# Kernel optimization log

Measured on AMD Instinct MI355X. Metric: run time of the kernel, lower is better.

The kernel has to match this reference:

```python
import jax, jax.numpy as jnp
import numpy as np

EPS = 1e-15          # min-norm clamp (matches torch min_norm)
BALL_EPS = 4e-3      # float32 Poincare ball boundary eps
C = 1.0              # curvature for every layer


def _artanh(x):
    x = jnp.clip(x, -1.0 + 1e-7, 1.0 - 1e-7)
    return 0.5 * jnp.log((1.0 + x) / (1.0 - x))


def _norm(x):
    return jnp.maximum(jnp.linalg.norm(x, axis=-1, keepdims=True), EPS)


def proj(x, c):
    # clip points to stay inside the ball of radius (1-eps)/sqrt(c)
    n = _norm(x)
    maxnorm = (1.0 - BALL_EPS) / jnp.sqrt(c)
    return jnp.where(n > maxnorm, x / n * maxnorm, x)


def expmap0(u, c):
    sc = jnp.sqrt(c)
    n = _norm(u)
    return jnp.tanh(sc * n) * u / (sc * n)


def logmap0(p, c):
    sc = jnp.sqrt(c)
    n = _norm(p)
    return _artanh(sc * n) * p / (sc * n)


def mobius_add(x, y, c):
    x2 = jnp.sum(x * x, axis=-1, keepdims=True)
    y2 = jnp.sum(y * y, axis=-1, keepdims=True)
    xy = jnp.sum(x * y, axis=-1, keepdims=True)
    num = (1.0 + 2.0 * c * xy + c * y2) * x + (1.0 - c * x2) * y
    den = 1.0 + 2.0 * c * xy + (c ** 2) * x2 * y2
    return num / jnp.maximum(den, EPS)


def mobius_matvec(W, x, c):
    # torch HypLinear: mx = x @ W.T
    sc = jnp.sqrt(c)
    xn = _norm(x)
    mx = x @ W.T
    mxn = _norm(mx)
    res = jnp.tanh(mxn / xn * _artanh(sc * xn)) * mx / (mxn * sc)
    zero = jnp.all(mx == 0.0, axis=-1, keepdims=True)
    return jnp.where(zero, jnp.zeros((), dtype=res.dtype), res)


def hgc_layer(h, src, dst, w, W, b, c_in, c_out, n_nodes):
    # HypLinear
    mv = proj(mobius_matvec(W, h, c_in), c_in)
    hb = proj(expmap0(b[None, :], c_in), c_in)
    h = proj(mobius_add(mv, hb, c_in), c_in)
    # HypAgg: spmm in the tangent space at the origin
    xt = logmap0(h, c_in)                                  # [N, D]
    msg = w[:, None] * xt[src]                             # [E, D]
    agg = jax.ops.segment_sum(msg, dst, num_segments=n_nodes)
    h = proj(expmap0(agg, c_in), c_in)
    # HypAct: relu in tangent space, re-map with c_out
    xt = jax.nn.relu(logmap0(h, c_in))
    return proj(expmap0(xt, c_out), c_out)


def setup_inputs() -> dict:
    key = jax.random.key(0)
    k = jax.random.split(key, 8)
    N, E, F, D = 80000, 1280000, 256, 64
    x = jax.random.normal(k[0], (N, F), dtype=jnp.float32)
    src = jax.random.randint(k[1], (E,), 0, N)
    dst = jax.random.randint(k[2], (E,), 0, N)
    edge_weight = jax.random.uniform(k[3], (E,), dtype=jnp.float32)
    W1 = jax.random.normal(k[4], (D, F), dtype=jnp.float32) / np.sqrt(F)
    b1 = jax.random.normal(k[5], (D,), dtype=jnp.float32) * 0.01
    W2 = jax.random.normal(k[6], (D, D), dtype=jnp.float32) / np.sqrt(D)
    b2 = jax.random.normal(k[7], (D,), dtype=jnp.float32) * 0.01
    return {"x": x, "src": src, "dst": dst, "edge_weight": edge_weight,
            "W1": W1, "b1": b1, "W2": W2, "b2": b2}


def reference(x, src, dst, edge_weight, W1, b1, W2, b2):
    n_nodes = x.shape[0]
    # encode(): proj_tan0 is identity on the Poincare ball
    h = proj(expmap0(x, C), C)
    h = hgc_layer(h, src, dst, edge_weight, W1, b1, C, C, n_nodes)
    h = hgc_layer(h, src, dst, edge_weight, W2, b2, C, C, n_nodes)
    return h
```

## Files before the change

kernel.cpp:

```cpp
#include <hip/hip_runtime.h>


#define EPSV 1e-15f
#define MAXN 0.996f

typedef unsigned short bfu;
typedef __attribute__((ext_vector_type(8))) short v8s;
typedef __attribute__((ext_vector_type(4))) float v4f;

__device__ __forceinline__ bfu f2b(float f) {
    unsigned int u;
    __builtin_memcpy(&u, &f, sizeof(u));
    u += 0x7fffu + ((u >> 16) & 1u);
    return (bfu)(u >> 16);
}

__device__ __forceinline__ float b2f(bfu s) {
    unsigned int u = ((unsigned int)s) << 16;
    float f;
    __builtin_memcpy(&f, &u, sizeof(f));
    return f;
}

__device__ __forceinline__ float uplo(unsigned int u) {
    unsigned int v = u << 16; float f;
    __builtin_memcpy(&f, &v, sizeof(f)); return f;
}
__device__ __forceinline__ float uphi(unsigned int u) {
    unsigned int v = u & 0xffff0000u; float f;
    __builtin_memcpy(&f, &v, sizeof(f)); return f;
}

__device__ __forceinline__ v8s cvt8(const float* f) {
    v8s r;
#pragma unroll
    for (int j = 0; j < 8; ++j) r[j] = (short)f2b(f[j]);
    return r;
}

__device__ __forceinline__ float i2f(int i) {
    float f; __builtin_memcpy(&f, &i, sizeof(f)); return f;
}
__device__ __forceinline__ int f2i(float f) {
    int i; __builtin_memcpy(&i, &f, sizeof(i)); return i;
}

__device__ __forceinline__ float wredsum(float v) {
#pragma unroll
    for (int o = 32; o > 0; o >>= 1) v += __shfl_xor(v, o, 64);
    return v;
}

__device__ __forceinline__ float artanh_(float x) {
    x = fminf(fmaxf(x, -1.0f + 1e-7f), 1.0f - 1e-7f);
    return 0.5f * logf((1.0f + x) / (1.0f - x));
}

__device__ __forceinline__ float mobius_tail(float mx, float xn, float hb, float y2) {
    float mxn2 = wredsum(mx * mx);
    unsigned long long nz = __ballot(mx != 0.0f);
    float mxn = fmaxf(sqrtf(mxn2), EPSV);
    float rt = tanhf(mxn / xn * artanh_(xn));
    float mv, x2s;
    if (nz != 0ull) {
        mv = (rt / mxn) * mx;
        float mvn = fmaxf(fabsf(rt), EPSV);
        if (mvn > MAXN) mv *= MAXN / mvn;
        float cn = fminf(mvn, MAXN);
        x2s = cn * cn;
    } else { mv = 0.0f; x2s = 0.0f; }
    float xy = wredsum(mv * hb);
    float ca = 1.0f + 2.0f * xy + y2;
    float cb = 1.0f - x2s;
    float den = fmaxf(1.0f + 2.0f * xy + x2s * y2, EPSV);
    float hj = (ca * mv + cb * hb) / den;
    float hn = fmaxf(sqrtf(wredsum(hj * hj)), EPSV);
    if (hn > MAXN) { hj *= MAXN / hn; hn = MAXN; }
    return (artanh_(hn) / hn) * hj;
}

__device__ __forceinline__ float agg_transform(float a, float* xn_out) {
    float n = fmaxf(sqrtf(wredsum(a * a)), EPSV);
    float th = tanhf(n);
    float g = th / n;
    float nh = fmaxf(th, EPSV);
    if (nh > MAXN) { g *= MAXN / nh; nh = MAXN; }
    float h = g * a;
    float t = fmaxf((artanh_(nh) / nh) * h, 0.0f);
    float n2 = fmaxf(sqrtf(wredsum(t * t)), EPSV);
    float th2 = tanhf(n2);
    float g2 = th2 / n2;
    float nh2 = fmaxf(th2, EPSV);
    if (nh2 > MAXN) { g2 *= MAXN / nh2; nh2 = MAXN; }
    *xn_out = nh2;
    return g2 * t;
}

__device__ __forceinline__ float bias_point(const float* bv, int lane, float* y2) {
    float b = bv[lane];
    float bn = fmaxf(sqrtf(wredsum(b * b)), EPSV);
    float gs = tanhf(bn) / bn;
    float hbn = fmaxf(tanhf(bn), EPSV);
    if (hbn > MAXN) gs *= MAXN / hbn;
    float hb = gs * b;
    *y2 = wredsum(hb * hb);
    return hb;
}

__global__ __launch_bounds__(256) void hgA_zero(float* __restrict__ p, int n4) {
    const float4 z = make_float4(0.f, 0.f, 0.f, 0.f);
    int stride = gridDim.x * blockDim.x;
    for (int i = blockIdx.x * blockDim.x + threadIdx.x; i < n4; i += stride)
        ((float4*)p)[i] = z;
}

__global__ __launch_bounds__(256) void hgA_prep(
    int* __restrict__ deg, int N,
    const float* __restrict__ W1, const float* __restrict__ W2,
    bfu* __restrict__ w1b, bfu* __restrict__ w2b, int NW1, int NW2)
{
    const int b = blockIdx.x, tid = threadIdx.x;
    if (b < 128) {
        for (int i = b * 256 + tid; i < N; i += 128 * 256) deg[i] = 0;
    } else if (b < 128 + (NW1 + 255) / 256) {
        int i = (b - 128) * 256 + tid;
        if (i < NW1) w1b[i] = f2b(W1[i]);
    } else {
        for (int i = tid; i < NW2; i += 256) w2b[i] = f2b(W2[i]);
    }
}

__device__ __forceinline__ void layer1_body(
    int bid, int tid, const float* __restrict__ x, const bfu* __restrict__ w1b,
    const float* __restrict__ b1v, bfu* __restrict__ xtb, int N)
{
    const int lane = tid & 63, wv = tid >> 6;
    const int nodeBase = (bid * 4 + wv) * 16;
    if (nodeBase >= N) return;

    float y2;
    float hb = bias_point(b1v, lane, &y2);
    float hbv[4];
#pragma unroll
    for (int t = 0; t < 4; ++t) hbv[t] = __shfl(hb, (lane & 15) + 16 * t);

    const int m = lane & 15, q = lane >> 4;
    v4f acc0 = {0,0,0,0}, acc1 = {0,0,0,0}, acc2 = {0,0,0,0}, acc3 = {0,0,0,0};
    float usq = 0.0f;

    const float* arow = x + (size_t)(nodeBase + m) * 256 + q * 8;
    const bfu* wrow = w1b + (size_t)m * 256 + q * 8;
#pragma unroll
    for (int s = 0; s < 8; ++s) {
        float af[8];
        *(float4*)(af)     = *(const float4*)(arow + s * 32);
        *(float4*)(af + 4) = *(const float4*)(arow + s * 32 + 4);
#pragma unroll
        for (int j = 0; j < 8; ++j) usq = fmaf(af[j], af[j], usq);
        v8s a = cvt8(af);
        const bfu* wb = wrow + s * 32;
        acc0 = __builtin_amdgcn_mfma_f32_16x16x32_bf16(a, *(const v8s*)(wb), acc0, 0, 0, 0);
        acc1 = __builtin_amdgcn_mfma_f32_16x16x32_bf16(a, *(const v8s*)(wb + 16 * 256), acc1, 0, 0, 0);
        acc2 = __builtin_amdgcn_mfma_f32_16x16x32_bf16(a, *(const v8s*)(wb + 32 * 256), acc2, 0, 0, 0);
        acc3 = __builtin_amdgcn_mfma_f32_16x16x32_bf16(a, *(const v8s*)(wb + 48 * 256), acc3, 0, 0, 0);
    }
    usq += __shfl_xor(usq, 16, 64);
    usq += __shfl_xor(usq, 32, 64);

    float P[4], Q[4];
#pragma unroll
    for (int r = 0; r < 4; ++r) {
        float s2 = acc0[r]*acc0[r] + acc1[r]*acc1[r] + acc2[r]*acc2[r] + acc3[r]*acc3[r];
        float sh = acc0[r]*hbv[0] + acc1[r]*hbv[1] + acc2[r]*hbv[2] + acc3[r]*hbv[3];
#pragma unroll
        for (int o = 1; o < 16; o <<= 1) {
            s2 += __shfl_xor(s2, o, 64);
            sh += __shfl_xor(sh, o, 64);
        }
        float usq_r = __shfl(usq, q * 4 + r);
        float n  = fmaxf(sqrtf(usq_r), EPSV);
        float th = tanhf(n);
        float gamma = th / n;
        float xn = fmaxf(th, EPSV);
        if (xn > MAXN) { gamma *= MAXN / xn; xn = MAXN; }
        float mxn = fmaxf(gamma * sqrtf(s2), EPSV);
        float rt  = tanhf(mxn / xn * artanh_(xn));
        float k1, x2s, xy;
        if (s2 != 0.0f) {
            k1 = (rt / mxn) * gamma;
            float mvn = fmaxf(fabsf(rt), EPSV);
            if (mvn > MAXN) k1 *= MAXN / mvn;
            float cn = fminf(mvn, MAXN);
            x2s = cn * cn;
            xy  = k1 * sh;
        } else { k1 = 0.0f; x2s = 0.0f; xy = 0.0f; }
        float ca = 1.0f + 2.0f * xy + y2;
        float cb = 1.0f - x2s;
        float den = fmaxf(1.0f + 2.0f * xy + x2s * y2, EPSV);
        float hn2 = ca*ca*x2s + 2.0f*ca*cb*xy + cb*cb*y2;
        float hn = fmaxf(sqrtf(hn2) / den, EPSV);
        float hs = 1.0f;
        if (hn > MAXN) { hs = MAXN / hn; hn = MAXN; }
        float lam = artanh_(hn) / hn;
        P[r] = lam * hs * ca * k1 / den;
        Q[r] = lam * hs * cb / den;
    }
#pragma unroll
    for (int r = 0; r < 4; ++r) {
        bfu* orow = xtb + (size_t)(nodeBase + q * 4 + r) * 64 + m;
        orow[ 0] = f2b(P[r] * acc0[r] + Q[r] * hbv[0]);
        orow[16] = f2b(P[r] * acc1[r] + Q[r] * hbv[1]);
        orow[32] = f2b(P[r] * acc2[r] + Q[r] * hbv[2]);
        orow[48] = f2b(P[r] * acc3[r] + Q[r] * hbv[3]);
    }
}

__global__ __launch_bounds__(256) void hgA_zero_i32(int* __restrict__ p, int n) {
    int stride = gridDim.x * blockDim.x;
    for (int i = blockIdx.x * blockDim.x + threadIdx.x; i < n; i += stride) p[i] = 0;
}

__global__ __launch_bounds__(256) void hgA_count(
    const int* __restrict__ dst, int* __restrict__ deg, int E) {
    int stride = gridDim.x * blockDim.x;
    for (int e = blockIdx.x * blockDim.x + threadIdx.x; e < E; e += stride)
        atomicAdd(&deg[dst[e]], 1);
}

__global__ __launch_bounds__(256) void hgA_count_rank_l1(
    const int* __restrict__ dst, int* __restrict__ deg, int* __restrict__ rank,
    int E, int nf, int nl,
    const float* __restrict__ x, const bfu* __restrict__ w1b,
    const float* __restrict__ b1v, bfu* __restrict__ xtb, int N)
{
    const int b = blockIdx.x;
    const int mn = nf < nl ? nf : nl;
    bool isC; int idx;
    if (b < 2 * mn) { isC = !(b & 1); idx = b >> 1; }
    else            { isC = (nf > nl); idx = mn + (b - 2 * mn); }
    if (isC) {
        int e0 = (idx * 256 + threadIdx.x) * 4;
        if (e0 + 4 <= E) {
            int4 d4 = *(const int4*)(dst + e0);
            int4 r4;
            r4.x = atomicAdd(&deg[d4.x], 1);
            r4.y = atomicAdd(&deg[d4.y], 1);
            r4.z = atomicAdd(&deg[d4.z], 1);
            r4.w = atomicAdd(&deg[d4.w], 1);
            *(int4*)(rank + e0) = r4;
        } else if (e0 < E) {
            for (int e = e0; e < E; ++e) rank[e] = atomicAdd(&deg[dst[e]], 1);
        }
    } else {
        layer1_body(idx, threadIdx.x, x, w1b, b1v, xtb, N);
    }
}

__global__ __launch_bounds__(256) void hgA_scan1(
    const int* __restrict__ deg, int* __restrict__ rowst,
    int* __restrict__ bsum, int N)
{
    __shared__ int wsum[4];
    const int tid = threadIdx.x, lane = tid & 63, wv = tid >> 6;
    const int base = blockIdx.x * 1024 + tid * 4;
    int v0 = 0, v1 = 0, v2 = 0, v3 = 0;
    if (base + 4 <= N) {
        int4 d4 = *(const int4*)(deg + base);
        v0 = d4.x; v1 = d4.y; v2 = d4.z; v3 = d4.w;
    } else {
        if (base + 0 < N) v0 = deg[base + 0];
        if (base + 1 < N) v1 = deg[base + 1];
        if (base + 2 < N) v2 = deg[base + 2];
        if (base + 3 < N) v3 = deg[base + 3];
    }
    const int tsum = v0 + v1 + v2 + v3;
    int incl = tsum;
#pragma unroll
    for (int o = 1; o < 64; o <<= 1) {
        int nb = __shfl_up(incl, o, 64);
        if (lane >= o) incl += nb;
    }
    if (lane == 63) wsum[wv] = incl;
    __syncthreads();
    int add = 0;
#pragma unroll
    for (int w = 0; w < 4; ++w) { int s = wsum[w]; if (w < wv) add += s; }
    const int excl = add + incl - tsum;
    const int e0 = excl, e1 = e0 + v0, e2 = e1 + v1, e3 = e2 + v2;
    if (base + 4 <= N) {
        *(int4*)(rowst + base) = make_int4(e0, e1, e2, e3);
    } else {
        if (base + 0 < N) rowst[base + 0] = e0;
        if (base + 1 < N) rowst[base + 1] = e1;
        if (base + 2 < N) rowst[base + 2] = e2;
        if (base + 3 < N) rowst[base + 3] = e3;
    }
    if (tid == 255) bsum[blockIdx.x] = add + incl;
}

__global__ __launch_bounds__(64) void hgA_scan2(
    int* __restrict__ bsum, int* __restrict__ tot, int NB)
{
    const int lane = threadIdx.x;
    int run = 0;
    for (int b = 0; b < NB; b += 64) {
        int i = b + lane;
        int v = (i < NB) ? bsum[i] : 0;
        int incl = v;
#pragma unroll
        for (int o = 1; o < 64; o <<= 1) {
            int nb = __shfl_up(incl, o, 64);
            if (lane >= o) incl += nb;
        }
        if (i < NB) bsum[i] = run + incl - v;
        run += __shfl(incl, 63);
    }
    if (lane == 0) *tot = run;
}

__global__ __launch_bounds__(256) void hgA_scan3(
    int* __restrict__ rowst, const int* __restrict__ bsum, int N)
{
    const int base = blockIdx.x * 1024 + threadIdx.x * 4;
    const int off = bsum[blockIdx.x];
    if (base + 4 <= N) {
        int4 r = *(int4*)(rowst + base);
        r.x += off; r.y += off; r.z += off; r.w += off;
        *(int4*)(rowst + base) = r;
    } else {
        for (int i = base; i < N; ++i) rowst[i] += off;
    }
}

__global__ __launch_bounds__(1024) void hgA_scan_l1(
    const int* __restrict__ deg, int* __restrict__ row_start,
    int* __restrict__ cursor, int N,
    const float* __restrict__ x, const bfu* __restrict__ w1b,
    const float* __restrict__ b1v, bfu* __restrict__ xtb, int NL)
{
    if (blockIdx.x != 0) {
        int vb = (blockIdx.x - 1) * 4 + (threadIdx.x >> 8);
        if (vb < NL) layer1_body(vb, threadIdx.x & 255, x, w1b, b1v, xtb, N);
        return;
    }
    __shared__ int wsum[16];
    __shared__ int srun;
    const int tid = threadIdx.x, lane = tid & 63, wv = tid >> 6;
    if (tid == 0) srun = 0;
    __syncthreads();
    for (int base = 0; base < N; base += 1024) {
        int i = base + tid;
        int v = (i < N) ? deg[i] : 0;
        int incl = v;
#pragma unroll
        for (int o = 1; o < 64; o <<= 1) {
            int nbr = __shfl_up(incl, o, 64);
            if (lane >= o) incl += nbr;
        }
        if (lane == 63) wsum[wv] = incl;
        __syncthreads();
        int add = 0;
#pragma unroll
        for (int w = 0; w < 16; ++w) { int s = wsum[w]; if (w < wv) add += s; }
        int excl = srun + add + incl - v;
        if (i < N) { row_start[i] = excl; cursor[i] = excl; }
        __syncthreads();
        if (tid == 1023) srun += add + incl;
        __syncthreads();
    }
    if (tid == 0) row_start[N] = srun;
}

__global__ __launch_bounds__(256) void hgA_fill_layer1(
    const int* __restrict__ src, const int* __restrict__ dst,
    const float* __restrict__ ew, int* __restrict__ cursor,
    int2* __restrict__ csr, int E, int fillBlocks,
    const float* __restrict__ x, const bfu* __restrict__ w1b,
    const float* __restrict__ b1v, bfu* __restrict__ xtb, int N)
{
    const int b = blockIdx.x;
    if (b < fillBlocks) {
        int stride = fillBlocks * blockDim.x;
        for (int e = b * blockDim.x + threadIdx.x; e < E; e += stride) {
            int d = dst[e];
            int slot = atomicAdd(&cursor[d], 1);
            csr[slot] = make_int2(src[e], f2i(ew[e]));
        }
    } else {
        layer1_body(b - fillBlocks, threadIdx.x, x, w1b, b1v, xtb, N);
    }
}

__global__ __launch_bounds__(256) void hgA_fillr_layer1(
    const int* __restrict__ src, const int* __restrict__ dst,
    const float* __restrict__ ew, const int* __restrict__ rank,
    const int* __restrict__ row_start, int2* __restrict__ csr,
    int E, int nf, int nl, int l1off,
    const float* __restrict__ x, const bfu* __restrict__ w1b,
    const float* __restrict__ b1v, bfu* __restrict__ xtb, int N)
{
    const int b = blockIdx.x;
    const int mn = nf < nl ? nf : nl;
    bool isFill; int idx;
    if (b < 2 * mn) { isFill = !(b & 1); idx = b >> 1; }
    else            { isFill = (nf > nl); idx = mn + (b - 2 * mn); }
    if (isFill) {
        int e0 = (idx * 256 + threadIdx.x) * 4;
        if (e0 + 4 <= E) {
            int4  d4 = *(const int4*)(dst + e0);
            int4  s4 = *(const int4*)(src + e0);
            int4  r4 = *(const int4*)(rank + e0);
            float4 w4 = *(const float4*)(ew + e0);
            csr[row_start[d4.x] + r4.x] = make_int2(s4.x, f2i(w4.x));
            csr[row_start[d4.y] + r4.y] = make_int2(s4.y, f2i(w4.y));
            csr[row_start[d4.z] + r4.z] = make_int2(s4.z, f2i(w4.z));
            csr[row_start[d4.w] + r4.w] = make_int2(s4.w, f2i(w4.w));
        } else if (e0 < E) {
            for (int e = e0; e < E; ++e)
                csr[row_start[dst[e]] + rank[e]] = make_int2(src[e], f2i(ew[e]));
        }
    } else {
        layer1_body(l1off + idx, threadIdx.x, x, w1b, b1v, xtb, N);
    }
}

#define GACC_QUAD(T64, CSR, N0, N1, LANE, T0, T1, T2, T3)                      \
    {                                                                          \
        const int sl_ = (LANE) & 15, p_ = (LANE) >> 4;                         \
        float a0x=0.f,a0y=0.f,a0z=0.f,a0w=0.f;                                 \
        float a1x=0.f,a1y=0.f,a1z=0.f,a1w=0.f;                                 \
        float a2x=0.f,a2y=0.f,a2z=0.f,a2w=0.f;                                 \
        float a3x=0.f,a3y=0.f,a3z=0.f,a3w=0.f;                                 \
        for (int base = (N0); base < (N1); base += 64) {                       \
            int cnt = (N1) - base; if (cnt > 64) cnt = 64;                     \
            int sL = 0; float wL = 0.0f;                                       \
            if ((LANE) < cnt) { int2 rec = (CSR)[base + (LANE)];               \
                                sL = rec.x; wL = i2f(rec.y); }                 \
            int j = 0;                                                         \
            for (; j + 16 <= cnt; j += 16) {                                   \
                int   s0 = __shfl(sL, j      + p_, 64);                        \
                int   s1 = __shfl(sL, j +  4 + p_, 64);                        \
                int   s2 = __shfl(sL, j +  8 + p_, 64);                        \
                int   s3 = __shfl(sL, j + 12 + p_, 64);                        \
                float w0 = __shfl(wL, j      + p_, 64);                        \
                float w1 = __shfl(wL, j +  4 + p_, 64);                        \
                float w2 = __shfl(wL, j +  8 + p_, 64);                        \
                float w3 = __shfl(wL, j + 12 + p_, 64);                        \
                uint2 u0 = (T64)[(size_t)s0 * 16 + sl_];                       \
                uint2 u1 = (T64)[(size_t)s1 * 16 + sl_];                       \
                uint2 u2 = (T64)[(size_t)s2 * 16 + sl_];                       \
                uint2 u3 = (T64)[(size_t)s3 * 16 + sl_];                       \
                a0x = fmaf(w0, uplo(u0.x), a0x); a0y = fmaf(w0, uphi(u0.x), a0y); \
                a0z = fmaf(w0, uplo(u0.y), a0z); a0w = fmaf(w0, uphi(u0.y), a0w); \
                a1x = fmaf(w1, uplo(u1.x), a1x); a1y = fmaf(w1, uphi(u1.x), a1y); \
                a1z = fmaf(w1, uplo(u1.y), a1z); a1w = fmaf(w1, uphi(u1.y), a1w); \
                a2x = fmaf(w2, uplo(u2.x), a2x); a2y = fmaf(w2, uphi(u2.x), a2y); \
                a2z = fmaf(w2, uplo(u2.y), a2z); a2w = fmaf(w2, uphi(u2.y), a2w); \
                a3x = fmaf(w3, uplo(u3.x), a3x); a3y = fmaf(w3, uphi(u3.x), a3y); \
                a3z = fmaf(w3, uplo(u3.y), a3z); a3w = fmaf(w3, uphi(u3.y), a3w); \
            }                                                                  \
            for (; j + 8 <= cnt; j += 8) {                                     \
                int   s0 = __shfl(sL, j     + p_, 64);                         \
                int   s1 = __shfl(sL, j + 4 + p_, 64);                         \
                float w0 = __shfl(wL, j     + p_, 64);                         \
                float w1 = __shfl(wL, j + 4 + p_, 64);                         \
                uint2 u0 = (T64)[(size_t)s0 * 16 + sl_];                       \
                uint2 u1 = (T64)[(size_t)s1 * 16 + sl_];                       \
                a0x = fmaf(w0, uplo(u0.x), a0x); a0y = fmaf(w0, uphi(u0.x), a0y); \
                a0z = fmaf(w0, uplo(u0.y), a0z); a0w = fmaf(w0, uphi(u0.y), a0w); \
                a1x = fmaf(w1, uplo(u1.x), a1x); a1y = fmaf(w1, uphi(u1.x), a1y); \
                a1z = fmaf(w1, uplo(u1.y), a1z); a1w = fmaf(w1, uphi(u1.y), a1w); \
            }                                                                  \
            for (; j < cnt; j += 4) {         \
                int   s = __shfl(sL, j + p_, 64);                              \
                float w = __shfl(wL, j + p_, 64);                              \
                uint2 u = (T64)[(size_t)s * 16 + sl_];                         \
                a0x = fmaf(w, uplo(u.x), a0x); a0y = fmaf(w, uphi(u.x), a0y);  \
                a0z = fmaf(w, uplo(u.y), a0z); a0w = fmaf(w, uphi(u.y), a0w);  \
            }                                                                  \
        }                                                                      \
        T0 = (a0x + a1x) + (a2x + a3x);                                        \
        T1 = (a0y + a1y) + (a2y + a3y);                                        \
        T2 = (a0z + a1z) + (a2z + a3z);                                        \
        T3 = (a0w + a1w) + (a2w + a3w);                                        \
        T0 += __shfl_xor(T0, 16, 64); T0 += __shfl_xor(T0, 32, 64);            \
        T1 += __shfl_xor(T1, 16, 64); T1 += __shfl_xor(T1, 32, 64);            \
        T2 += __shfl_xor(T2, 16, 64); T2 += __shfl_xor(T2, 32, 64);            \
        T3 += __shfl_xor(T3, 16, 64); T3 += __shfl_xor(T3, 32, 64);            \
    }

__global__ __launch_bounds__(256) void hgA_gather(
    const int* __restrict__ row_start, const int2* __restrict__ csr,
    const bfu* __restrict__ xtb, float* __restrict__ agg, int N) {
    const int lane = threadIdx.x & 63, wv = threadIdx.x >> 6;
    const int d = blockIdx.x * 4 + wv;
    if (d >= N) return;
    const uint2* t64 = (const uint2*)xtb;
    const int n0 = row_start[d], n1 = row_start[d + 1];
    float t0, t1, t2, t3;
    GACC_QUAD(t64, csr, n0, n1, lane, t0, t1, t2, t3);
    if ((lane >> 4) == 0)
        *(float4*)(agg + (size_t)d * 64 + 4 * (lane & 15)) =
            make_float4(t0, t1, t2, t3);
}

__global__ __launch_bounds__(256) void hgA_gather_out(
    const int* __restrict__ row_start, const int2* __restrict__ csr,
    const bfu* __restrict__ xtb2, float* __restrict__ out, int N) {
    const int lane = threadIdx.x & 63, wv = threadIdx.x >> 6;
    const int d = blockIdx.x * 4 + wv;
    if (d >= N) return;
    const uint2* t64 = (const uint2*)xtb2;
    const int n0 = row_start[d], n1 = row_start[d + 1];
    float t0, t1, t2, t3;
    GACC_QUAD(t64, csr, n0, n1, lane, t0, t1, t2, t3);
    float ssq = t0*t0 + t1*t1 + t2*t2 + t3*t3;
#pragma unroll
    for (int o = 1; o < 16; o <<= 1) ssq += __shfl_xor(ssq, o, 64);
    float n  = fmaxf(sqrtf(ssq), EPSV);
    float th = tanhf(n);
    float g  = th / n;
    float nh = fmaxf(th, EPSV);
    if (nh > MAXN) { g *= MAXN / nh; nh = MAXN; }
    float lamg = (artanh_(nh) / nh) * g;
    float r0 = fmaxf(lamg * t0, 0.0f);
    float r1 = fmaxf(lamg * t1, 0.0f);
    float r2 = fmaxf(lamg * t2, 0.0f);
    float r3 = fmaxf(lamg * t3, 0.0f);
    float tsq = r0*r0 + r1*r1 + r2*r2 + r3*r3;
#pragma unroll
    for (int o = 1; o < 16; o <<= 1) tsq += __shfl_xor(tsq, o, 64);
    float n2  = fmaxf(sqrtf(tsq), EPSV);
    float th2 = tanhf(n2);
    float g2  = th2 / n2;
    float nh2 = fmaxf(th2, EPSV);
    if (nh2 > MAXN) g2 *= MAXN / nh2;
    if ((lane >> 4) == 0)
        *(float4*)(out + (size_t)d * 64 + 4 * (lane & 15)) =
            make_float4(g2 * r0, g2 * r1, g2 * r2, g2 * r3);
}

__global__ __launch_bounds__(256) void hgA_layer2_mfma(
    const float* __restrict__ agg,
    const bfu* __restrict__ w2b,
    const float* __restrict__ b2v,
    bfu* __restrict__ xtb2, int N)
{
    const int tid = threadIdx.x, lane = tid & 63, wv = tid >> 6;
    const int nodeBase = (blockIdx.x * 4 + wv) * 16;
    if (nodeBase >= N) return;

    float y2;
    float hb = bias_point(b2v, lane, &y2);
    float hbv[4];
#pragma unroll
    for (int t = 0; t < 4; ++t) hbv[t] = __shfl(hb, (lane & 15) + 16 * t);

    const int m = lane & 15, q = lane >> 4;
    const bool rowok = (nodeBase + m) < N;

    float af0[8], af1[8];
    const float* arow = agg + (size_t)(nodeBase + m) * 64 + q * 8;
    if (rowok) {
        *(float4*)(af0)     = *(const float4*)(arow);
        *(float4*)(af0 + 4) = *(const float4*)(arow + 4);
        *(float4*)(af1)     = *(const float4*)(arow + 32);
        *(float4*)(af1 + 4) = *(const float4*)(arow + 36);
    } else {
#pragma unroll
        for (int j = 0; j < 8; ++j) { af0[j] = 0.0f; af1[j] = 0.0f; }
    }
    float asq = 0.0f;
#pragma unroll
    for (int j = 0; j < 8; ++j) {
        asq = fmaf(af0[j], af0[j], asq);
        asq = fmaf(af1[j], af1[j], asq);
    }
    asq += __shfl_xor(asq, 16, 64);
    asq += __shfl_xor(asq, 32, 64);

    float n  = fmaxf(sqrtf(asq), EPSV);
    float th = tanhf(n);
    float g  = th / n;
    float nh = fmaxf(th, EPSV);
    if (nh > MAXN) { g *= MAXN / nh; nh = MAXN; }
    float lamg = (artanh_(nh) / nh) * g;
    float t0[8], t1[8], tsq = 0.0f;
#pragma unroll
    for (int j = 0; j < 8; ++j) {
        t0[j] = fmaxf(lamg * af0[j], 0.0f);
        t1[j] = fmaxf(lamg * af1[j], 0.0f);
        tsq = fmaf(t0[j], t0[j], tsq);
        tsq = fmaf(t1[j], t1[j], tsq);
    }
    tsq += __shfl_xor(tsq, 16, 64);
    tsq += __shfl_xor(tsq, 32, 64);
    float n2  = fmaxf(sqrtf(tsq), EPSV);
    float th2 = tanhf(n2);
    float g2  = th2 / n2;
    float nh2 = fmaxf(th2, EPSV);
    if (nh2 > MAXN) { g2 *= MAXN / nh2; nh2 = MAXN; }
    float xn_m = nh2;
    float x0[8], x1[8];
#pragma unroll
    for (int j = 0; j < 8; ++j) { x0[j] = g2 * t0[j]; x1[j] = g2 * t1[j]; }
    v8s a0 = cvt8(x0), a1 = cvt8(x1);

    v4f acc0 = {0,0,0,0}, acc1 = {0,0,0,0}, acc2 = {0,0,0,0}, acc3 = {0,0,0,0};
    {
        const bfu* wb;
        wb = w2b + (size_t)(m     ) * 64 + q * 8;
        acc0 = __builtin_amdgcn_mfma_f32_16x16x32_bf16(a0, *(const v8s*)(wb),      acc0, 0, 0, 0);
        acc0 = __builtin_amdgcn_mfma_f32_16x16x32_bf16(a1, *(const v8s*)(wb + 32), acc0, 0, 0, 0);
        wb = w2b + (size_t)(m + 16) * 64 + q * 8;
        acc1 = __builtin_amdgcn_mfma_f32_16x16x32_bf16(a0, *(const v8s*)(wb),      acc1, 0, 0, 0);
        acc1 = __builtin_amdgcn_mfma_f32_16x16x32_bf16(a1, *(const v8s*)(wb + 32), acc1, 0, 0, 0);
        wb = w2b + (size_t)(m + 32) * 64 + q * 8;
        acc2 = __builtin_amdgcn_mfma_f32_16x16x32_bf16(a0, *(const v8s*)(wb),      acc2, 0, 0, 0);
        acc2 = __builtin_amdgcn_mfma_f32_16x16x32_bf16(a1, *(const v8s*)(wb + 32), acc2, 0, 0, 0);
        wb = w2b + (size_t)(m + 48) * 64 + q * 8;
        acc3 = __builtin_amdgcn_mfma_f32_16x16x32_bf16(a0, *(const v8s*)(wb),      acc3, 0, 0, 0);
        acc3 = __builtin_amdgcn_mfma_f32_16x16x32_bf16(a1, *(const v8s*)(wb + 32), acc3, 0, 0, 0);
    }

    float P[4], Q[4];
#pragma unroll
    for (int r = 0; r < 4; ++r) {
        float s2 = acc0[r]*acc0[r] + acc1[r]*acc1[r] + acc2[r]*acc2[r] + acc3[r]*acc3[r];
        float sh = acc0[r]*hbv[0] + acc1[r]*hbv[1] + acc2[r]*hbv[2] + acc3[r]*hbv[3];
#pragma unroll
        for (int o = 1; o < 16; o <<= 1) {
            s2 += __shfl_xor(s2, o, 64);
            sh += __shfl_xor(sh, o, 64);
        }
        float xn = __shfl(xn_m, q * 4 + r);
        float mxn = fmaxf(sqrtf(s2), EPSV);
        float rt  = tanhf(mxn / xn * artanh_(xn));
        float k1, x2s, xy;
        if (s2 != 0.0f) {
            k1 = rt / mxn;
            float mvn = fmaxf(fabsf(rt), EPSV);
            if (mvn > MAXN) k1 *= MAXN / mvn;
            float cn = fminf(mvn, MAXN);
            x2s = cn * cn;
            xy  = k1 * sh;
        } else { k1 = 0.0f; x2s = 0.0f; xy = 0.0f; }
        float ca = 1.0f + 2.0f * xy + y2;
        float cb = 1.0f - x2s;
        float den = fmaxf(1.0f + 2.0f * xy + x2s * y2, EPSV);
        float hn2 = ca*ca*x2s + 2.0f*ca*cb*xy + cb*cb*y2;
        float hn = fmaxf(sqrtf(hn2) / den, EPSV);
        float hs = 1.0f;
        if (hn > MAXN) { hs = MAXN / hn; hn = MAXN; }
        float lam = artanh_(hn) / hn;
        P[r] = lam * hs * ca * k1 / den;
        Q[r] = lam * hs * cb / den;
    }
#pragma unroll
    for (int r = 0; r < 4; ++r) {
        int ri = nodeBase + q * 4 + r;
        if (ri < N) {
            bfu* orow = xtb2 + (size_t)ri * 64 + m;
            orow[ 0] = f2b(P[r] * acc0[r] + Q[r] * hbv[0]);
            orow[16] = f2b(P[r] * acc1[r] + Q[r] * hbv[1]);
            orow[32] = f2b(P[r] * acc2[r] + Q[r] * hbv[2]);
            orow[48] = f2b(P[r] * acc3[r] + Q[r] * hbv[3]);
        }
    }
}

__global__ __launch_bounds__(256) void hgA_layer1_fp32(
    const float* __restrict__ x, const float* __restrict__ W1,
    const float* __restrict__ b1v, float* __restrict__ xt, int N)
{
    const int tid = threadIdx.x, lane = tid & 63, wv = tid >> 6;
    const int nodeBase = (blockIdx.x * 4 + wv) * 16;
    if (nodeBase >= N) return;
    float y2;
    float hb = bias_point(b1v, lane, &y2);
    float hbv[4];
#pragma unroll
    for (int t = 0; t < 4; ++t) hbv[t] = __shfl(hb, (lane & 15) + 16 * t);
    const int m = lane & 15, q = lane >> 4;
    v4f acc0 = {0,0,0,0}, acc1 = {0,0,0,0}, acc2 = {0,0,0,0}, acc3 = {0,0,0,0};
    float usq = 0.0f;
    const float* arow = x + (size_t)(nodeBase + m) * 256 + q * 8;
#pragma unroll
    for (int s = 0; s < 8; ++s) {
        float af[8];
        *(float4*)(af)     = *(const float4*)(arow + s * 32);
        *(float4*)(af + 4) = *(const float4*)(arow + s * 32 + 4);
#pragma unroll
        for (int j = 0; j < 8; ++j) usq = fmaf(af[j], af[j], usq);
        v8s a = cvt8(af);
        const float* wbase = W1 + (size_t)m * 256 + s * 32 + q * 8;
        float wf[8];
        *(float4*)(wf) = *(const float4*)(wbase);  *(float4*)(wf+4) = *(const float4*)(wbase+4);
        acc0 = __builtin_amdgcn_mfma_f32_16x16x32_bf16(a, cvt8(wf), acc0, 0, 0, 0);
        *(float4*)(wf) = *(const float4*)(wbase+16*256); *(float4*)(wf+4) = *(const float4*)(wbase+16*256+4);
        acc1 = __builtin_amdgcn_mfma_f32_16x16x32_bf16(a, cvt8(wf), acc1, 0, 0, 0);
        *(float4*)(wf) = *(const float4*)(wbase+32*256); *(float4*)(wf+4) = *(const float4*)(wbase+32*256+4);
        acc2 = __builtin_amdgcn_mfma_f32_16x16x32_bf16(a, cvt8(wf), acc2, 0, 0, 0);
        *(float4*)(wf) = *(const float4*)(wbase+48*256); *(float4*)(wf+4) = *(const float4*)(wbase+48*256+4);
        acc3 = __builtin_amdgcn_mfma_f32_16x16x32_bf16(a, cvt8(wf), acc3, 0, 0, 0);
    }
    usq += __shfl_xor(usq, 16, 64);
    usq += __shfl_xor(usq, 32, 64);
    float P[4], Q[4];
#pragma unroll
    for (int r = 0; r < 4; ++r) {
        float s2 = acc0[r]*acc0[r] + acc1[r]*acc1[r] + acc2[r]*acc2[r] + acc3[r]*acc3[r];
        float sh = acc0[r]*hbv[0] + acc1[r]*hbv[1] + acc2[r]*hbv[2] + acc3[r]*hbv[3];
#pragma unroll
        for (int o = 1; o < 16; o <<= 1) { s2 += __shfl_xor(s2, o, 64); sh += __shfl_xor(sh, o, 64); }
        float usq_r = __shfl(usq, q * 4 + r);
        float n  = fmaxf(sqrtf(usq_r), EPSV);
        float th = tanhf(n);
        float gamma = th / n;
        float xn = fmaxf(th, EPSV);
        if (xn > MAXN) { gamma *= MAXN / xn; xn = MAXN; }
        float mxn = fmaxf(gamma * sqrtf(s2), EPSV);
        float rt  = tanhf(mxn / xn * artanh_(xn));
        float k1, x2s, xy;
        if (s2 != 0.0f) {
            k1 = (rt / mxn) * gamma;
            float mvn = fmaxf(fabsf(rt), EPSV);
            if (mvn > MAXN) k1 *= MAXN / mvn;
            float cn = fminf(mvn, MAXN);
            x2s = cn * cn; xy = k1 * sh;
        } else { k1 = 0.0f; x2s = 0.0f; xy = 0.0f; }
        float ca = 1.0f + 2.0f * xy + y2;
        float cb = 1.0f - x2s;
        float den = fmaxf(1.0f + 2.0f * xy + x2s * y2, EPSV);
        float hn2 = ca*ca*x2s + 2.0f*ca*cb*xy + cb*cb*y2;
        float hn = fmaxf(sqrtf(hn2) / den, EPSV);
        float hs = 1.0f;
        if (hn > MAXN) { hs = MAXN / hn; hn = MAXN; }
        float lam = artanh_(hn) / hn;
        P[r] = lam * hs * ca * k1 / den;
        Q[r] = lam * hs * cb / den;
    }
#pragma unroll
    for (int r = 0; r < 4; ++r) {
        float* orow = xt + (size_t)(nodeBase + q * 4 + r) * 64 + m;
        orow[ 0] = P[r] * acc0[r] + Q[r] * hbv[0];
        orow[16] = P[r] * acc1[r] + Q[r] * hbv[1];
        orow[32] = P[r] * acc2[r] + Q[r] * hbv[2];
        orow[48] = P[r] * acc3[r] + Q[r] * hbv[3];
    }
}

__global__ __launch_bounds__(256) void hgA_scatter(
    const int* __restrict__ src, const int* __restrict__ dst,
    const float* __restrict__ ew,
    const float* __restrict__ xt, float* __restrict__ agg, int E)
{
    const int lane = threadIdx.x & 63;
    const long long wid = ((long long)blockIdx.x * blockDim.x + threadIdx.x) >> 6;
    const long long nw = ((long long)gridDim.x * blockDim.x) >> 6;
    for (long long e = wid; e < E; e += nw) {
        int s = src[e], d = dst[e];
        atomicAdd(&agg[(size_t)d * 64 + lane], ew[e] * xt[(size_t)s * 64 + lane]);
    }
}

__global__ __launch_bounds__(256) void hgA_layer2_fb(
    const float* __restrict__ agg,
    const float* __restrict__ W2, const float* __restrict__ b2v,
    float* __restrict__ xt2, int N)
{
    const int lane = threadIdx.x & 63, wv = threadIdx.x >> 6;
    float y2;
    float hb = bias_point(b2v, lane, &y2);
    const int nw = gridDim.x * 4;
    for (int i = blockIdx.x * 4 + wv; i < N; i += nw) {
        float a = agg[(size_t)i * 64 + lane];
        float xn;
        float x2 = agg_transform(a, &xn);
        float acc = 0.0f;
        const float* Wrow = W2 + (size_t)lane * 64;
        for (int s = 0; s < 64; ++s)
            acc = fmaf(__shfl(x2, s), Wrow[s], acc);
        float o = mobius_tail(acc, xn, hb, y2);
        xt2[(size_t)i * 64 + lane] = o;
    }
}

__global__ __launch_bounds__(256) void hgA_final_fb(
    const float* __restrict__ agg, float* __restrict__ out, int N)
{
    const int lane = threadIdx.x & 63, wv = threadIdx.x >> 6;
    const int nw = gridDim.x * 4;
    for (int i = blockIdx.x * 4 + wv; i < N; i += nw) {
        float a = agg[(size_t)i * 64 + lane];
        float xn;
        float o = agg_transform(a, &xn);
        out[(size_t)i * 64 + lane] = o;
    }
}

extern "C" void kernel_launch(void* const* d_in, const int* in_sizes, int n_in,
                              void* d_out, int out_size, void* d_ws, size_t ws_size,
                              hipStream_t stream)
{
    const float* x  = (const float*)d_in[0];
    const int* src  = (const int*)d_in[1];
    const int* dst  = (const int*)d_in[2];
    const float* ew = (const float*)d_in[3];
    const float* W1 = (const float*)d_in[4];
    const float* b1 = (const float*)d_in[5];
    const float* W2 = (const float*)d_in[6];
    const float* b2 = (const float*)d_in[7];

    const int Dd = in_sizes[5];
    const int Ff = in_sizes[4] / Dd;
    const int N  = in_sizes[0] / Ff;
    const int E  = in_sizes[1];
    const int NW1 = Dd * Ff;
    const int NW2 = Dd * Dd;

    float* out = (float*)d_out;
    float* agg = (float*)d_out;

    const int NB = (N + 1023) / 1024;

    bfu*  xtb    = (bfu*)d_ws;
    size_t xtb_b = (size_t)N * Dd * 2;
    int*  deg    = (int*)((char*)d_ws + xtb_b);
    int*  rowst  = deg + N;
    int*  cursor = rowst + (N + 1);
    int*  rank   = cursor + N;
    int*  bsum   = rank + E;

    size_t wA_off = (xtb_b + ((size_t)(3 * N + 1) + (size_t)E + (size_t)NB) * 4 + 15) & ~(size_t)15;
    bfu* w1bA = (bfu*)((char*)d_ws + wA_off);
    bfu* w2bA = w1bA + NW1;
    size_t csr_offA = (wA_off + (size_t)(NW1 + NW2) * 2 + 7) & ~(size_t)7;
    const size_t needA = csr_offA + (size_t)E * 8;

    size_t wB_off = (xtb_b + (size_t)(3 * N + 1) * 4 + 15) & ~(size_t)15;
    bfu* w1bB = (bfu*)((char*)d_ws + wB_off);
    bfu* w2bB = w1bB + NW1;
    size_t csr_offB = (wB_off + (size_t)(NW1 + NW2) * 2 + 7) & ~(size_t)7;
    const size_t needB = csr_offB + (size_t)E * 8;

    const int blkT = (N + 63) / 64;
    const int blkG = (N + 3) / 4;
    const int blkE4 = (E + 1023) / 1024;
    const int prepG = 128 + (NW1 + 255) / 256 + 1;
    const int n4 = (N * Dd) / 4;

    if (ws_size >= needA) {
        int2* csr = (int2*)((char*)d_ws + csr_offA);
        int L1C = blkT < 780 ? blkT : 780;
        int L1F = blkT - L1C;
        hgA_prep        <<<prepG, 256, 0, stream>>>(deg, N, W1, W2, w1bA, w2bA, NW1, NW2);
        hgA_count_rank_l1<<<blkE4 + L1C, 256, 0, stream>>>(
            dst, deg, rank, E, blkE4, L1C, x, w1bA, b1, xtb, N);
        hgA_scan1       <<<NB, 256, 0, stream>>>(deg, rowst, bsum, N);
        hgA_scan2       <<<1,   64, 0, stream>>>(bsum, rowst + N, NB);
        hgA_scan3       <<<NB, 256, 0, stream>>>(rowst, bsum, N);
        hgA_fillr_layer1<<<blkE4 + L1F, 256, 0, stream>>>(
            src, dst, ew, rank, rowst, csr, E, blkE4, L1F, L1C,
            x, w1bA, b1, xtb, N);
        hgA_gather     <<<blkG, 256, 0, stream>>>(rowst, csr, xtb, agg, N);
        hgA_layer2_mfma<<<blkT, 256, 0, stream>>>(agg, w2bA, b2, xtb, N);
        hgA_gather_out <<<blkG, 256, 0, stream>>>(rowst, csr, xtb, out, N);
    } else if (ws_size >= needB) {
        int2* csr = (int2*)((char*)d_ws + csr_offB);
        const int fillBlocks = 2048;
        hgA_prep       <<<prepG, 256, 0, stream>>>(deg, N, W1, W2, w1bB, w2bB, NW1, NW2);
        hgA_count      <<<2048, 256, 0, stream>>>(dst, deg, E);
        hgA_scan_l1    <<<1,   1024, 0, stream>>>(
            deg, rowst, cursor, N, x, w1bB, b1, xtb, 0);
        hgA_fill_layer1<<<fillBlocks + blkT, 256, 0, stream>>>(
            src, dst, ew, cursor, csr, E, fillBlocks, x, w1bB, b1, xtb, N);
        hgA_gather     <<<blkG, 256, 0, stream>>>(rowst, csr, xtb, agg, N);
        hgA_layer2_mfma<<<blkT, 256, 0, stream>>>(agg, w2bB, b2, xtb, N);
        hgA_gather_out <<<blkG, 256, 0, stream>>>(rowst, csr, xtb, out, N);
    } else {
        float* xt_fb  = (float*)d_out;
        float* agg_fb = (float*)d_ws;
        hgA_layer1_fp32<<<blkT, 256, 0, stream>>>(x, W1, b1, xt_fb, N);
        hgA_zero     <<<1024,  256, 0, stream>>>(agg_fb, n4);
        hgA_scatter  <<<16384, 256, 0, stream>>>(src, dst, ew, xt_fb, agg_fb, E);
        hgA_layer2_fb<<<2048,  256, 0, stream>>>(agg_fb, W2, b2, xt_fb, N);
        hgA_zero     <<<1024,  256, 0, stream>>>(agg_fb, n4);
        hgA_scatter  <<<16384, 256, 0, stream>>>(src, dst, ew, xt_fb, agg_fb, E);
        hgA_final_fb <<<2048,  256, 0, stream>>>(agg_fb, out, N);
    }
}
```

Baseline: 334.8 us.

## Pre-convert x to bf16 alongside degree counting and spread layer-1 GEMM across scan and fill

Adds a new top path, used when the workspace is large enough, that converts the fp32 feature matrix to bf16 and precomputes per-node squared norms inside the edge-counting kernel. The layer-1 MFMA work then reads the half-size bf16 copy and is split between the scan kernel and the CSR fill kernel, instead of being interleaved with the atomic counting pass. The aim is to overlap the dense layer-1 work with latency-bound scan and fill phases and to halve the bytes the GEMM reads. In exchange it writes and re-reads an extra N×256 bf16 buffer and needs a larger workspace.

After: 333.4 us. Within noise of the previous version (-0.4%).

```diff
diff --git a/kernel.cpp b/kernel.cpp
--- a/kernel.cpp
+++ b/kernel.cpp
@@ -130,43 +130,10 @@
     }
 }
 
-__device__ __forceinline__ void layer1_body(
-    int bid, int tid, const float* __restrict__ x, const bfu* __restrict__ w1b,
-    const float* __restrict__ b1v, bfu* __restrict__ xtb, int N)
-{
-    const int lane = tid & 63, wv = tid >> 6;
-    const int nodeBase = (bid * 4 + wv) * 16;
-    if (nodeBase >= N) return;
-
-    float y2;
-    float hb = bias_point(b1v, lane, &y2);
-    float hbv[4];
-#pragma unroll
-    for (int t = 0; t < 4; ++t) hbv[t] = __shfl(hb, (lane & 15) + 16 * t);
-
-    const int m = lane & 15, q = lane >> 4;
-    v4f acc0 = {0,0,0,0}, acc1 = {0,0,0,0}, acc2 = {0,0,0,0}, acc3 = {0,0,0,0};
-    float usq = 0.0f;
-
-    const float* arow = x + (size_t)(nodeBase + m) * 256 + q * 8;
-    const bfu* wrow = w1b + (size_t)m * 256 + q * 8;
-#pragma unroll
-    for (int s = 0; s < 8; ++s) {
-        float af[8];
-        *(float4*)(af)     = *(const float4*)(arow + s * 32);
-        *(float4*)(af + 4) = *(const float4*)(arow + s * 32 + 4);
-#pragma unroll
-        for (int j = 0; j < 8; ++j) usq = fmaf(af[j], af[j], usq);
-        v8s a = cvt8(af);
-        const bfu* wb = wrow + s * 32;
-        acc0 = __builtin_amdgcn_mfma_f32_16x16x32_bf16(a, *(const v8s*)(wb), acc0, 0, 0, 0);
-        acc1 = __builtin_amdgcn_mfma_f32_16x16x32_bf16(a, *(const v8s*)(wb + 16 * 256), acc1, 0, 0, 0);
-        acc2 = __builtin_amdgcn_mfma_f32_16x16x32_bf16(a, *(const v8s*)(wb + 32 * 256), acc2, 0, 0, 0);
-        acc3 = __builtin_amdgcn_mfma_f32_16x16x32_bf16(a, *(const v8s*)(wb + 48 * 256), acc3, 0, 0, 0);
-    }
-    usq += __shfl_xor(usq, 16, 64);
-    usq += __shfl_xor(usq, 32, 64);
-
+__device__ __forceinline__ void layer1_tail(
+    int nodeBase, int m, int q, float usq, const float* hbv, float y2,
+    v4f acc0, v4f acc1, v4f acc2, v4f acc3, bfu* __restrict__ xtb)
+{
     float P[4], Q[4];
 #pragma unroll
     for (int r = 0; r < 4; ++r) {
@@ -215,6 +182,78 @@
     }
 }
 
+__device__ __forceinline__ void layer1_body(
+    int bid, int tid, const float* __restrict__ x, const bfu* __restrict__ w1b,
+    const float* __restrict__ b1v, bfu* __restrict__ xtb, int N)
+{
+    const int lane = tid & 63, wv = tid >> 6;
+    const int nodeBase = (bid * 4 + wv) * 16;
+    if (nodeBase >= N) return;
+
+    float y2;
+    float hb = bias_point(b1v, lane, &y2);
+    float hbv[4];
+#pragma unroll
+    for (int t = 0; t < 4; ++t) hbv[t] = __shfl(hb, (lane & 15) + 16 * t);
+
+    const int m = lane & 15, q = lane >> 4;
+    v4f acc0 = {0,0,0,0}, acc1 = {0,0,0,0}, acc2 = {0,0,0,0}, acc3 = {0,0,0,0};
+    float usq = 0.0f;
+
+    const float* arow = x + (size_t)(nodeBase + m) * 256 + q * 8;
+    const bfu* wrow = w1b + (size_t)m * 256 + q * 8;
+#pragma unroll
+    for (int s = 0; s < 8; ++s) {
+        float af[8];
+        *(float4*)(af)     = *(const float4*)(arow + s * 32);
+        *(float4*)(af + 4) = *(const float4*)(arow + s * 32 + 4);
+#pragma unroll
+        for (int j = 0; j < 8; ++j) usq = fmaf(af[j], af[j], usq);
+        v8s a = cvt8(af);
+        const bfu* wb = wrow + s * 32;
+        acc0 = __builtin_amdgcn_mfma_f32_16x16x32_bf16(a, *(const v8s*)(wb), acc0, 0, 0, 0);
+        acc1 = __builtin_amdgcn_mfma_f32_16x16x32_bf16(a, *(const v8s*)(wb + 16 * 256), acc1, 0, 0, 0);
+        acc2 = __builtin_amdgcn_mfma_f32_16x16x32_bf16(a, *(const v8s*)(wb + 32 * 256), acc2, 0, 0, 0);
+        acc3 = __builtin_amdgcn_mfma_f32_16x16x32_bf16(a, *(const v8s*)(wb + 48 * 256), acc3, 0, 0, 0);
+    }
+    usq += __shfl_xor(usq, 16, 64);
+    usq += __shfl_xor(usq, 32, 64);
+    layer1_tail(nodeBase, m, q, usq, hbv, y2, acc0, acc1, acc2, acc3, xtb);
+}
+
+__device__ __forceinline__ void layer1b_body(
+    int bid, int tid, const bfu* __restrict__ xb, const float* __restrict__ usqt,
+    const bfu* __restrict__ w1b, const float* __restrict__ b1v,
+    bfu* __restrict__ xtb, int N)
+{
+    const int lane = tid & 63, wv = tid >> 6;
+    const int nodeBase = (bid * 4 + wv) * 16;
+    if (nodeBase >= N) return;
+
+    float y2;
+    float hb = bias_point(b1v, lane, &y2);
+    float hbv[4];
+#pragma unroll
+    for (int t = 0; t < 4; ++t) hbv[t] = __shfl(hb, (lane & 15) + 16 * t);
+
+    const int m = lane & 15, q = lane >> 4;
+    v4f acc0 = {0,0,0,0}, acc1 = {0,0,0,0}, acc2 = {0,0,0,0}, acc3 = {0,0,0,0};
+    const float usq = usqt[nodeBase + m];
+
+    const bfu* arow = xb + (size_t)(nodeBase + m) * 256 + q * 8;
+    const bfu* wrow = w1b + (size_t)m * 256 + q * 8;
+#pragma unroll
+    for (int s = 0; s < 8; ++s) {
+        v8s a = *(const v8s*)(arow + s * 32);
+        const bfu* wb = wrow + s * 32;
+        acc0 = __builtin_amdgcn_mfma_f32_16x16x32_bf16(a, *(const v8s*)(wb), acc0, 0, 0, 0);
+        acc1 = __builtin_amdgcn_mfma_f32_16x16x32_bf16(a, *(const v8s*)(wb + 16 * 256), acc1, 0, 0, 0);
+        acc2 = __builtin_amdgcn_mfma_f32_16x16x32_bf16(a, *(const v8s*)(wb + 32 * 256), acc2, 0, 0, 0);
+        acc3 = __builtin_amdgcn_mfma_f32_16x16x32_bf16(a, *(const v8s*)(wb + 48 * 256), acc3, 0, 0, 0);
+    }
+    layer1_tail(nodeBase, m, q, usq, hbv, y2, acc0, acc1, acc2, acc3, xtb);
+}
+
 __global__ __launch_bounds__(256) void hgA_zero_i32(int* __restrict__ p, int n) {
     int stride = gridDim.x * blockDim.x;
     for (int i = blockIdx.x * blockDim.x + threadIdx.x; i < n; i += stride) p[i] = 0;
@@ -256,10 +295,65 @@
     }
 }
 
+__global__ __launch_bounds__(256) void hgA_count_xcvt(
+    const int* __restrict__ dst, int* __restrict__ deg, int* __restrict__ rank,
+    int E, int nf,
+    const float* __restrict__ x, bfu* __restrict__ xb, float* __restrict__ usqt,
+    int nc, int N)
+{
+    const int b = blockIdx.x;
+    const int mn = nf < nc ? nf : nc;
+    bool isC; int idx;
+    if (b < 2 * mn) { isC = !(b & 1); idx = b >> 1; }
+    else            { isC = (nf > nc); idx = mn + (b - 2 * mn); }
+    if (isC) {
+        int e0 = (idx * 256 + threadIdx.x) * 4;
+        if (e0 + 4 <= E) {
+            int4 d4 = *(const int4*)(dst + e0);
+            int4 r4;
+            r4.x = atomicAdd(&deg[d4.x], 1);
+            r4.y = atomicAdd(&deg[d4.y], 1);
+            r4.z = atomicAdd(&deg[d4.z], 1);
+            r4.w = atomicAdd(&deg[d4.w], 1);
+            *(int4*)(rank + e0) = r4;
+        } else if (e0 < E) {
+            for (int e = e0; e < E; ++e) rank[e] = atomicAdd(&deg[dst[e]], 1);
+        }
+    } else {
+        const int lane = threadIdx.x & 63, wv = threadIdx.x >> 6;
+        const int nodeBase = (idx * 4 + wv) * 16;
+        if (nodeBase >= N) return;
+        const int m = lane & 15, q = lane >> 4;
+        const float* arow = x + (size_t)(nodeBase + m) * 256 + q * 8;
+        bfu* orow = xb + (size_t)(nodeBase + m) * 256 + q * 8;
+        float usq = 0.0f;
+#pragma unroll
+        for (int s = 0; s < 8; ++s) {
+            float af[8];
+            *(float4*)(af)     = *(const float4*)(arow + s * 32);
+            *(float4*)(af + 4) = *(const float4*)(arow + s * 32 + 4);
+#pragma unroll
+            for (int j = 0; j < 8; ++j) usq = fmaf(af[j], af[j], usq);
+            *(v8s*)(orow + s * 32) = cvt8(af);
+        }
+        usq += __shfl_xor(usq, 16, 64);
+        usq += __shfl_xor(usq, 32, 64);
+        if (lane < 16 && nodeBase + lane < N) usqt[nodeBase + lane] = usq;
+    }
+}
+
 __global__ __launch_bounds__(256) void hgA_scan1(
     const int* __restrict__ deg, int* __restrict__ rowst,
-    int* __restrict__ bsum, int N)
-{
+    int* __restrict__ bsum, int N, int NBr,
+    const bfu* __restrict__ xb, const float* __restrict__ usqt,
+    const bfu* __restrict__ w1b, const float* __restrict__ b1v,
+    bfu* __restrict__ xtb, int NL)
+{
+    if (blockIdx.x >= NBr) {
+        int vb = blockIdx.x - NBr;
+        if (vb < NL) layer1b_body(vb, threadIdx.x, xb, usqt, w1b, b1v, xtb, N);
+        return;
+    }
     __shared__ int wsum[4];
     const int tid = threadIdx.x, lane = tid & 63, wv = tid >> 6;
     const int base = blockIdx.x * 1024 + tid * 4;
@@ -421,6 +515,40 @@
         }
     } else {
         layer1_body(l1off + idx, threadIdx.x, x, w1b, b1v, xtb, N);
+    }
+}
+
+__global__ __launch_bounds__(256) void hgA_fillr_l1b(
+    const int* __restrict__ src, const int* __restrict__ dst,
+    const float* __restrict__ ew, const int* __restrict__ rank,
+    const int* __restrict__ row_start, int2* __restrict__ csr,
+    int E, int nf, int nl, int l1off,
+    const bfu* __restrict__ xb, const float* __restrict__ usqt,
+    const bfu* __restrict__ w1b, const float* __restrict__ b1v,
+    bfu* __restrict__ xtb, int N)
+{
+    const int b = blockIdx.x;
+    const int mn = nf < nl ? nf : nl;
+    bool isFill; int idx;
+    if (b < 2 * mn) { isFill = !(b & 1); idx = b >> 1; }
+    else            { isFill = (nf > nl); idx = mn + (b - 2 * mn); }
+    if (isFill) {
+        int e0 = (idx * 256 + threadIdx.x) * 4;
+        if (e0 + 4 <= E) {
+            int4  d4 = *(const int4*)(dst + e0);
+            int4  s4 = *(const int4*)(src + e0);
+            int4  r4 = *(const int4*)(rank + e0);
+            float4 w4 = *(const float4*)(ew + e0);
+            csr[row_start[d4.x] + r4.x] = make_int2(s4.x, f2i(w4.x));
+            csr[row_start[d4.y] + r4.y] = make_int2(s4.y, f2i(w4.y));
+            csr[row_start[d4.z] + r4.z] = make_int2(s4.z, f2i(w4.z));
+            csr[row_start[d4.w] + r4.w] = make_int2(s4.w, f2i(w4.w));
+        } else if (e0 < E) {
+            for (int e = e0; e < E; ++e)
+                csr[row_start[dst[e]] + rank[e]] = make_int2(src[e], f2i(ew[e]));
+        }
+    } else {
+        layer1b_body(l1off + idx, threadIdx.x, xb, usqt, w1b, b1v, xtb, N);
     }
 }
 
@@ -824,19 +952,38 @@
 
     const int NB = (N + 1023) / 1024;
 
-    bfu*  xtb    = (bfu*)d_ws;
+    const int blkT = (N + 63) / 64;
+    const int blkG = (N + 3) / 4;
+    const int blkE4 = (E + 1023) / 1024;
+    const int prepG = 128 + (NW1 + 255) / 256 + 1;
+    const int n4 = (N * Dd) / 4;
+
     size_t xtb_b = (size_t)N * Dd * 2;
+    size_t xb_b  = (size_t)N * Ff * 2;
+    bfu*  xtb   = (bfu*)d_ws;
+    bfu*  xbA   = (bfu*)((char*)d_ws + xtb_b);
+    float* usqt = (float*)((char*)d_ws + xtb_b + xb_b);
+    size_t off1 = xtb_b + xb_b + (size_t)N * 4;
+    int*  degA1   = (int*)((char*)d_ws + off1);
+    int*  rowstA1 = degA1 + N;
+    int*  rankA1  = rowstA1 + (N + 1);
+    int*  bsumA1  = rankA1 + E;
+    size_t w1_offA1 = (off1 + ((size_t)(2 * N + 1) + (size_t)E + (size_t)NB) * 4 + 15) & ~(size_t)15;
+    bfu* w1bA1 = (bfu*)((char*)d_ws + w1_offA1);
+    bfu* w2bA1 = w1bA1 + NW1;
+    size_t csr_offA1 = (w1_offA1 + (size_t)(NW1 + NW2) * 2 + 7) & ~(size_t)7;
+    const size_t needA1 = csr_offA1 + (size_t)E * 8;
+
     int*  deg    = (int*)((char*)d_ws + xtb_b);
     int*  rowst  = deg + N;
     int*  cursor = rowst + (N + 1);
     int*  rank   = cursor + N;
     int*  bsum   = rank + E;
-
     size_t wA_off = (xtb_b + ((size_t)(3 * N + 1) + (size_t)E + (size_t)NB) * 4 + 15) & ~(size_t)15;
     bfu* w1bA = (bfu*)((char*)d_ws + wA_off);
     bfu* w2bA = w1bA + NW1;
     size_t csr_offA = (wA_off + (size_t)(NW1 + NW2) * 2 + 7) & ~(size_t)7;
-    const size_t needA = csr_offA + (size_t)E * 8;
+    const size_t needA2 = csr_offA + (size_t)E * 8;
 
     size_t wB_off = (xtb_b + (size_t)(3 * N + 1) * 4 + 15) & ~(size_t)15;
     bfu* w1bB = (bfu*)((char*)d_ws + wB_off);
@@ -844,20 +991,33 @@
     size_t csr_offB = (wB_off + (size_t)(NW1 + NW2) * 2 + 7) & ~(size_t)7;
     const size_t needB = csr_offB + (size_t)E * 8;
 
-    const int blkT = (N + 63) / 64;
-    const int blkG = (N + 3) / 4;
-    const int blkE4 = (E + 1023) / 1024;
-    const int prepG = 128 + (NW1 + 255) / 256 + 1;
-    const int n4 = (N * Dd) / 4;
-
-    if (ws_size >= needA) {
+    if (ws_size >= needA1) {
+        int2* csr = (int2*)((char*)d_ws + csr_offA1);
+        int L1S = blkT < 192 ? blkT : 192;
+        int L1F = blkT - L1S;
+        hgA_prep      <<<prepG, 256, 0, stream>>>(degA1, N, W1, W2, w1bA1, w2bA1, NW1, NW2);
+        hgA_count_xcvt<<<blkE4 + blkT, 256, 0, stream>>>(
+            dst, degA1, rankA1, E, blkE4, x, xbA, usqt, blkT, N);
+        hgA_scan1     <<<NB + L1S, 256, 0, stream>>>(
+            degA1, rowstA1, bsumA1, N, NB, xbA, usqt, w1bA1, b1, xtb, L1S);
+        hgA_scan2     <<<1, 64, 0, stream>>>(bsumA1, rowstA1 + N, NB);
+        hgA_scan3     <<<NB, 256, 0, stream>>>(rowstA1, bsumA1, N);
+        hgA_fillr_l1b <<<blkE4 + L1F, 256, 0, stream>>>(
+            src, dst, ew, rankA1, rowstA1, csr, E, blkE4, L1F, L1S,
+            xbA, usqt, w1bA1, b1, xtb, N);
+        hgA_gather     <<<blkG, 256, 0, stream>>>(rowstA1, csr, xtb, agg, N);
+        hgA_layer2_mfma<<<blkT, 256, 0, stream>>>(agg, w2bA1, b2, xtb, N);
+        hgA_gather_out <<<blkG, 256, 0, stream>>>(rowstA1, csr, xtb, out, N);
+    } else if (ws_size >= needA2) {
         int2* csr = (int2*)((char*)d_ws + csr_offA);
         int L1C = blkT < 780 ? blkT : 780;
         int L1F = blkT - L1C;
         hgA_prep        <<<prepG, 256, 0, stream>>>(deg, N, W1, W2, w1bA, w2bA, NW1, NW2);
         hgA_count_rank_l1<<<blkE4 + L1C, 256, 0, stream>>>(
             dst, deg, rank, E, blkE4, L1C, x, w1bA, b1, xtb, N);
-        hgA_scan1       <<<NB, 256, 0, stream>>>(deg, rowst, bsum, N);
+        hgA_scan1       <<<NB, 256, 0, stream>>>(deg, rowst, bsum, N, NB,
+                                                 (const bfu*)xtb, (const float*)deg,
+                                                 w1bA, b1, xtb, 0);
         hgA_scan2       <<<1,   64, 0, stream>>>(bsum, rowst + N, NB);
         hgA_scan3       <<<NB, 256, 0, stream>>>(rowst, bsum, N);
         hgA_fillr_layer1<<<blkE4 + L1F, 256, 0, stream>>>(
```
